# Performance work log

Hardware: AMD Instinct MI355X
Metric: run time of the kernel (lower is better)

## Reference

```python
import jax, jax.numpy as jnp
import numpy as np

B, N, D, O = 128, 256, 512, 512
EPS = 1e-5


def setup_inputs() -> dict:
    key = jax.random.key(0)
    ks = jax.random.split(key, 12)
    Observation = jax.random.normal(ks[0], (B, N, D), dtype=jnp.float32)
    mask = jax.random.bernoulli(ks[1], 0.7, (B, N))
    s = 0.02
    W1 = jax.random.normal(ks[2], (D, O), dtype=jnp.float32) * s
    W2 = jax.random.normal(ks[3], (O, O), dtype=jnp.float32) * s
    W3 = jax.random.normal(ks[4], (O, O), dtype=jnp.float32) * s
    g1 = 1.0 + 0.1 * jax.random.normal(ks[5], (D,), dtype=jnp.float32)
    b1 = 0.02 * jax.random.normal(ks[6], (D,), dtype=jnp.float32)
    g2 = 1.0 + 0.1 * jax.random.normal(ks[7], (O,), dtype=jnp.float32)
    b2 = 0.02 * jax.random.normal(ks[8], (O,), dtype=jnp.float32)
    g3 = 1.0 + 0.1 * jax.random.normal(ks[9], (O,), dtype=jnp.float32)
    b3 = 0.02 * jax.random.normal(ks[10], (O,), dtype=jnp.float32)
    return {"Observation": Observation, "mask": mask,
            "g1": g1, "b1": b1, "W1": W1,
            "g2": g2, "b2": b2, "W2": W2,
            "g3": g3, "b3": b3, "W3": W3}


def layer_norm(x, g, b):
    m = jnp.mean(x, axis=-1, keepdims=True)
    v = jnp.mean(jnp.square(x - m), axis=-1, keepdims=True)
    return (x - m) * jax.lax.rsqrt(v + EPS) * g + b


def reference(Observation, mask, g1, b1, W1, g2, b2, W2, g3, b3, W3):
    Bv, Nv, Dv = Observation.shape
    # _grant_at_least_one_valid: force element 0 valid if a row is all-invalid
    all_invalid = ~jnp.any(mask, axis=1)  # [B]
    mask = mask | (all_invalid[:, None] & (jnp.arange(Nv) == 0)[None, :])
    x = Observation.reshape(-1, Dv)  # [B*N, D]
    # Block 1: LN -> Linear (no bias) -> Tanh (dropout is eval identity)
    h1 = jnp.tanh(layer_norm(x, g1, b1) @ W1)
    # Block 2
    h2 = jnp.tanh(layer_norm(h1, g2, b2) @ W2)
    # Block 3 with residual input (h2 + h1), no activation
    o3 = layer_norm(h2 + h1, g3, b3) @ W3  # [B*N, O]
    fill = jnp.finfo(o3.dtype).min
    o3 = jnp.where(mask.reshape(-1, 1), o3, fill)
    out = jax.nn.softmax(o3.reshape(Bv, Nv, -1), axis=1)
    return jnp.nan_to_num(out, nan=0.0)
```

## Files before the change

kernel.cpp:

```cpp
#include <hip/hip_runtime.h>


#define RTOT 32768
#define NN   256

typedef _Float16 f16;
typedef __attribute__((ext_vector_type(4))) _Float16 f16x4;
typedef __attribute__((ext_vector_type(8))) _Float16 f16x8;
typedef __attribute__((ext_vector_type(4))) float f32x4;

#define EPS16 520
#define EPS32 516

__device__ __forceinline__ float fast_tanh(float x) {
  float e = __expf(2.f * x);
  return 1.f - 2.f * __builtin_amdgcn_rcpf(e + 1.f);
}
__device__ __forceinline__ void async_copy16(const void* g, void* l) {
  __builtin_amdgcn_global_load_lds(
      (const __attribute__((address_space(1))) unsigned int*)g,
      (__attribute__((address_space(3))) unsigned int*)l, 16, 0, 0);
}

__global__ void prep_w_kernel(const float* __restrict__ W1, const float* __restrict__ W2,
                              const float* __restrict__ W3, f16* __restrict__ WT) {
  int idx = blockIdx.x * 256 + threadIdx.x;
  int s   = idx >> 18;
  int rem = idx & 0x3FFFF;
  int o   = rem >> 9;
  int d   = rem & 511;
  const float* W = (s == 0) ? W1 : (s == 1) ? W2 : W3;
  WT[idx] = (f16)W[d * 512 + o];
}

__global__ __launch_bounds__(256) void ln1_kernel(const float* __restrict__ in,
                                                  const float* __restrict__ g,
                                                  const float* __restrict__ b,
                                                  f16* __restrict__ outA) {
  int wv = threadIdx.x >> 6, lane = threadIdx.x & 63;
  size_t row = (size_t)blockIdx.x * 4 + wv;
  const float* x = in + (row << 9);
  float4 v0 = *(const float4*)(x + lane * 4);
  float4 v1 = *(const float4*)(x + 256 + lane * 4);
  float s = v0.x + v0.y + v0.z + v0.w + v1.x + v1.y + v1.z + v1.w;
  float q = v0.x*v0.x + v0.y*v0.y + v0.z*v0.z + v0.w*v0.w
          + v1.x*v1.x + v1.y*v1.y + v1.z*v1.z + v1.w*v1.w;
  #pragma unroll
  for (int off = 1; off < 64; off <<= 1) {
    s += __shfl_xor(s, off, 64);
    q += __shfl_xor(q, off, 64);
  }
  float mean = s * (1.f / 512.f);
  float var  = q * (1.f / 512.f) - mean * mean;
  float inv  = 1.f / sqrtf(var + 1e-5f);
  float4 g0 = *(const float4*)(g + lane * 4);
  float4 b0 = *(const float4*)(b + lane * 4);
  float4 g1 = *(const float4*)(g + 256 + lane * 4);
  float4 b1 = *(const float4*)(b + 256 + lane * 4);
  f16x4 o0, o1;
  o0[0] = (f16)((v0.x - mean) * inv * g0.x + b0.x);
  o0[1] = (f16)((v0.y - mean) * inv * g0.y + b0.y);
  o0[2] = (f16)((v0.z - mean) * inv * g0.z + b0.z);
  o0[3] = (f16)((v0.w - mean) * inv * g0.w + b0.w);
  o1[0] = (f16)((v1.x - mean) * inv * g1.x + b1.x);
  o1[1] = (f16)((v1.y - mean) * inv * g1.y + b1.y);
  o1[2] = (f16)((v1.z - mean) * inv * g1.z + b1.z);
  o1[3] = (f16)((v1.w - mean) * inv * g1.w + b1.w);
  *(f16x4*)&outA[(row << 9) + lane * 4] = o0;
  *(f16x4*)&outA[(row << 9) + 256 + lane * 4] = o1;
}

template <int STAGE>
__global__ __launch_bounds__(512, 4) void fused_kernel(
    const f16* __restrict__ A, const f16* __restrict__ BT,
    const float* __restrict__ g, const float* __restrict__ b,
    f16* __restrict__ H1, f16* __restrict__ outH, float* __restrict__ outF) {
  __shared__ __align__(16) char smem[73728];
  __shared__ __align__(16) float2 sPart[512];
  __shared__ __align__(16) float2 sStat[64];
  f16* sA = (f16*)smem;
  f16* sB = (f16*)(smem + 8192);

  int t = threadIdx.x, lane = t & 63, wv = t >> 6;
  int row16 = lane & 15, quad = lane >> 4;
  int rBase = blockIdx.x * 64;
  int lr  = lane >> 3;
  int lcs = ((lane & 7) ^ (lane >> 3)) * 8;

  f32x4 acc[4][4] = {};

  for (int k0 = 0; k0 < 512; k0 += 64) {
    {
      const f16* ga = A + (((size_t)(rBase + wv * 8 + lr)) << 9) + k0 + lcs;
      async_copy16(ga, sA + (wv * 8) * 64);
    }
    #pragma unroll
    for (int p = 0; p < 8; ++p) {
      int r = wv * 64 + p * 8;
      const f16* gb = BT + (((size_t)(r + lr)) << 9) + k0 + lcs;
      async_copy16(gb, sB + r * 64);
    }
    __syncthreads();
    #pragma unroll
    for (int kk = 0; kk < 64; kk += 32) {
      int kb = kk >> 3;
      f16x8 af[4], bf[4];
      #pragma unroll
      for (int i = 0; i < 4; ++i) {
        int ar = i * 16 + row16;
        int br = wv * 64 + i * 16 + row16;
        af[i] = *(const f16x8*)&sA[ar * 64 + (((quad + kb) ^ (ar & 7)) << 3)];
        bf[i] = *(const f16x8*)&sB[br * 64 + (((quad + kb) ^ (br & 7)) << 3)];
      }
      #pragma unroll
      for (int mi = 0; mi < 4; ++mi)
        #pragma unroll
        for (int ni = 0; ni < 4; ++ni)
          acc[mi][ni] = __builtin_amdgcn_mfma_f32_16x16x32_f16(af[mi], bf[ni], acc[mi][ni], 0, 0, 0);
    }
    __syncthreads();
  }

  if constexpr (STAGE == 2) {
    float* sE = (float*)smem;
    #pragma unroll
    for (int half = 0; half < 2; ++half) {
      #pragma unroll
      for (int mi = 0; mi < 2; ++mi) {
        int rt = half * 2 + mi;
        #pragma unroll
        for (int ni = 0; ni < 4; ++ni) {
          int col = wv * 64 + ni * 16 + row16;
          #pragma unroll
          for (int rg = 0; rg < 4; ++rg)
            sE[(mi * 16 + quad * 4 + rg) * EPS32 + col] = acc[rt][ni][rg];
        }
      }
      __syncthreads();
      #pragma unroll
      for (int i = 0; i < 8; ++i) {
        int gi = t + i * 512;
        int row = gi >> 7, cg = (gi & 127) * 4;
        f32x4 v = *(const f32x4*)&sE[row * EPS32 + cg];
        *(f32x4*)&outF[(((size_t)(rBase + half * 32 + row)) << 9) + cg] = v;
      }
      __syncthreads();
    }
    return;
  } else {
    float gv[4], bv[4];
    #pragma unroll
    for (int ni = 0; ni < 4; ++ni) {
      int c = wv * 64 + ni * 16 + row16;
      gv[ni] = g[c]; bv[ni] = b[c];
    }

    f16* sH = (f16*)smem;
    if constexpr (STAGE == 1) {
      #pragma unroll
      for (int p = 0; p < 8; ++p) {
        const f16* gh = H1 + (((size_t)(rBase + wv * 8 + p)) << 9) + lane * 8;
        async_copy16(gh, sH + (wv * 8 + p) * 512);
      }
    }

    #pragma unroll
    for (int mi = 0; mi < 4; ++mi)
      #pragma unroll
      for (int ni = 0; ni < 4; ++ni)
        #pragma unroll
        for (int rg = 0; rg < 4; ++rg)
          acc[mi][ni][rg] = fast_tanh(acc[mi][ni][rg]);

    if constexpr (STAGE == 1) {
      __syncthreads();
      #pragma unroll
      for (int mi = 0; mi < 4; ++mi)
        #pragma unroll
        for (int ni = 0; ni < 4; ++ni) {
          int col = wv * 64 + ni * 16 + row16;
          #pragma unroll
          for (int rg = 0; rg < 4; ++rg)
            acc[mi][ni][rg] += (float)sH[(mi * 16 + quad * 4 + rg) * 512 + col];
        }
    }

    f16* sE = (f16*)smem;
    if constexpr (STAGE == 0) {
      #pragma unroll
      for (int mi = 0; mi < 4; ++mi)
        #pragma unroll
        for (int ni = 0; ni < 4; ++ni) {
          int col = wv * 64 + ni * 16 + row16;
          #pragma unroll
          for (int rg = 0; rg < 4; ++rg)
            sE[(mi * 16 + quad * 4 + rg) * EPS16 + col] = (f16)acc[mi][ni][rg];
        }
    }

    #pragma unroll
    for (int mi = 0; mi < 4; ++mi)
      #pragma unroll
      for (int rg = 0; rg < 4; ++rg) {
        float s = 0.f, q = 0.f;
        #pragma unroll
        for (int ni = 0; ni < 4; ++ni) {
          float v = acc[mi][ni][rg];
          s += v; q += v * v;
        }
        #pragma unroll
        for (int off = 1; off < 16; off <<= 1) {
          s += __shfl_xor(s, off, 16);
          q += __shfl_xor(q, off, 16);
        }
        if (row16 == 0)
          sPart[wv * 64 + mi * 16 + quad * 4 + rg] = make_float2(s, q);
      }
    __syncthreads();

    if (t < 64) {
      float s = 0.f, q = 0.f;
      #pragma unroll
      for (int w = 0; w < 8; ++w) {
        float2 p = sPart[w * 64 + t];
        s += p.x; q += p.y;
      }
      float mean = s * (1.f / 512.f);
      float var  = q * (1.f / 512.f) - mean * mean;
      sStat[t] = make_float2(mean, 1.f / sqrtf(var + 1e-5f));
    }
    if constexpr (STAGE == 0) {
      #pragma unroll
      for (int i = 0; i < 8; ++i) {
        int gi = t + i * 512;
        int row = gi >> 6, cg = (gi & 63) * 8;
        f16x8 v = *(const f16x8*)&sE[row * EPS16 + cg];
        *(f16x8*)&H1[(((size_t)(rBase + row)) << 9) + cg] = v;
      }
    }
    __syncthreads();

    #pragma unroll
    for (int mi = 0; mi < 4; ++mi)
      #pragma unroll
      for (int rg = 0; rg < 4; ++rg) {
        int row = mi * 16 + quad * 4 + rg;
        float2 st = sStat[row];
        #pragma unroll
        for (int ni = 0; ni < 4; ++ni) {
          int col = wv * 64 + ni * 16 + row16;
          sE[row * EPS16 + col] = (f16)((acc[mi][ni][rg] - st.x) * st.y * gv[ni] + bv[ni]);
        }
      }
    __syncthreads();

    #pragma unroll
    for (int i = 0; i < 8; ++i) {
      int gi = t + i * 512;
      int row = gi >> 6, cg = (gi & 63) * 8;
      f16x8 v = *(const f16x8*)&sE[row * EPS16 + cg];
      *(f16x8*)&outH[(((size_t)(rBase + row)) << 9) + cg] = v;
    }
  }
}

__global__ __launch_bounds__(256, 2) void softmax_kernel(const float* __restrict__ o3,
                                                         const int* __restrict__ mask,
                                                         float* __restrict__ out) {
  __shared__ float sz[NN * 64];
  __shared__ float sredm[4 * 64];
  __shared__ float sreds[4 * 64];
  __shared__ int   smask[NN];

  int b  = blockIdx.x >> 3;
  int oc = blockIdx.x & 7;
  int t  = threadIdx.x;
  int o_l = t & 63;
  int n_h = t >> 6;

  int mt = mask[b * NN + t];
  int any = __syncthreads_or(mt);
  smask[t] = (t == 0 && !any) ? 1 : mt;
  __syncthreads();

  const float* src = o3 + (((size_t)(b * NN)) << 9) + oc * 64;
  #pragma unroll 4
  for (int j = 0; j < 64; ++j) {
    int n = j * 4 + n_h;
    float v = src[((size_t)n << 9) + o_l];
    sz[n * 64 + o_l] = smask[n] ? v : -3.4e38f;
  }
  __syncthreads();

  float mx = -3.4e38f;
  #pragma unroll 8
  for (int i = 0; i < 64; ++i)
    mx = fmaxf(mx, sz[(n_h * 64 + i) * 64 + o_l]);
  sredm[n_h * 64 + o_l] = mx;
  __syncthreads();
  float m4 = fmaxf(fmaxf(sredm[o_l], sredm[64 + o_l]),
                   fmaxf(sredm[128 + o_l], sredm[192 + o_l]));

  float sm = 0.f;
  #pragma unroll 8
  for (int i = 0; i < 64; ++i)
    sm += __expf(sz[(n_h * 64 + i) * 64 + o_l] - m4);
  sreds[n_h * 64 + o_l] = sm;
  __syncthreads();
  float tot = sreds[o_l] + sreds[64 + o_l] + sreds[128 + o_l] + sreds[192 + o_l];
  float inv = 1.f / tot;

  float* dst = out + (((size_t)(b * NN)) << 9) + oc * 64;
  #pragma unroll 4
  for (int j = 0; j < 64; ++j) {
    int n = j * 4 + n_h;
    dst[((size_t)n << 9) + o_l] = __expf(sz[n * 64 + o_l] - m4) * inv;
  }
}

extern "C" void kernel_launch(void* const* d_in, const int* in_sizes, int n_in,
                              void* d_out, int out_size, void* d_ws, size_t ws_size,
                              hipStream_t stream) {
  const float* Obs = (const float*)d_in[0];
  const int*   msk = (const int*)d_in[1];
  const float* g1  = (const float*)d_in[2];
  const float* b1  = (const float*)d_in[3];
  const float* W1  = (const float*)d_in[4];
  const float* g2  = (const float*)d_in[5];
  const float* b2  = (const float*)d_in[6];
  const float* W2  = (const float*)d_in[7];
  const float* g3  = (const float*)d_in[8];
  const float* b3  = (const float*)d_in[9];
  const float* W3  = (const float*)d_in[10];
  float* out = (float*)d_out;

  char* ws = (char*)d_ws;
  const size_t MB = 1u << 20;
  f16*   Ah0 = (f16*)ws;
  f16*   Ah1 = (f16*)(ws + 32 * MB);
  f16*   H1h = (f16*)(ws + 64 * MB);
  float* Lg  = (float*)(ws + 64 * MB);
  f16*   WT  = (f16*)(ws + 128 * MB);

  prep_w_kernel<<<3072, 256, 0, stream>>>(W1, W2, W3, WT);
  ln1_kernel<<<8192, 256, 0, stream>>>(Obs, g1, b1, Ah0);
  fused_kernel<0><<<512, 512, 0, stream>>>(Ah0, WT,          g2, b2, H1h, Ah1, nullptr);
  fused_kernel<1><<<512, 512, 0, stream>>>(Ah1, WT + 262144, g3, b3, H1h, Ah0, nullptr);
  fused_kernel<2><<<512, 512, 0, stream>>>(Ah0, WT + 524288, nullptr, nullptr, nullptr, nullptr, Lg);
  softmax_kernel<<<1024, 256, 0, stream>>>(Lg, msk, out);
}
```

Measured before the change: 303.8 us.

## Fuse LN1 and all three GEMM stages into one persistent-row mega kernel

Replaces the separate LN1 kernel and three per-stage fused GEMM kernels with a single kernel. Each block keeps its 64-row activation tile resident in LDS across all three layers, holds h1 in registers as f16 for the residual, and streams weights through a double-buffered 32-wide K slice. The final logits are written as f16 instead of f32 to halve softmax input traffic. This removes the global round trips for intermediate activations and the extra launches, at the cost of more LDS per block (occupancy 2 instead of 4), higher register pressure, and reduced precision of the logits.

```diff
diff --git a/kernel.cpp b/kernel.cpp
--- a/kernel.cpp
+++ b/kernel.cpp
@@ -1,16 +1,13 @@
 #include <hip/hip_runtime.h>
 
 
-#define RTOT 32768
-#define NN   256
+#define NN 256
 
 typedef _Float16 f16;
+typedef __attribute__((ext_vector_type(2))) _Float16 f16x2;
 typedef __attribute__((ext_vector_type(4))) _Float16 f16x4;
 typedef __attribute__((ext_vector_type(8))) _Float16 f16x8;
 typedef __attribute__((ext_vector_type(4))) float f32x4;
-
-#define EPS16 520
-#define EPS32 516
 
 __device__ __forceinline__ float fast_tanh(float x) {
   float e = __expf(2.f * x);
@@ -33,238 +30,208 @@
   WT[idx] = (f16)W[d * 512 + o];
 }
 
-__global__ __launch_bounds__(256) void ln1_kernel(const float* __restrict__ in,
-                                                  const float* __restrict__ g,
-                                                  const float* __restrict__ b,
-                                                  f16* __restrict__ outA) {
-  int wv = threadIdx.x >> 6, lane = threadIdx.x & 63;
-  size_t row = (size_t)blockIdx.x * 4 + wv;
-  const float* x = in + (row << 9);
-  float4 v0 = *(const float4*)(x + lane * 4);
-  float4 v1 = *(const float4*)(x + 256 + lane * 4);
-  float s = v0.x + v0.y + v0.z + v0.w + v1.x + v1.y + v1.z + v1.w;
-  float q = v0.x*v0.x + v0.y*v0.y + v0.z*v0.z + v0.w*v0.w
-          + v1.x*v1.x + v1.y*v1.y + v1.z*v1.z + v1.w*v1.w;
-  #pragma unroll
-  for (int off = 1; off < 64; off <<= 1) {
-    s += __shfl_xor(s, off, 64);
-    q += __shfl_xor(q, off, 64);
-  }
-  float mean = s * (1.f / 512.f);
-  float var  = q * (1.f / 512.f) - mean * mean;
-  float inv  = 1.f / sqrtf(var + 1e-5f);
-  float4 g0 = *(const float4*)(g + lane * 4);
-  float4 b0 = *(const float4*)(b + lane * 4);
-  float4 g1 = *(const float4*)(g + 256 + lane * 4);
-  float4 b1 = *(const float4*)(b + 256 + lane * 4);
-  f16x4 o0, o1;
-  o0[0] = (f16)((v0.x - mean) * inv * g0.x + b0.x);
-  o0[1] = (f16)((v0.y - mean) * inv * g0.y + b0.y);
-  o0[2] = (f16)((v0.z - mean) * inv * g0.z + b0.z);
-  o0[3] = (f16)((v0.w - mean) * inv * g0.w + b0.w);
-  o1[0] = (f16)((v1.x - mean) * inv * g1.x + b1.x);
-  o1[1] = (f16)((v1.y - mean) * inv * g1.y + b1.y);
-  o1[2] = (f16)((v1.z - mean) * inv * g1.z + b1.z);
-  o1[3] = (f16)((v1.w - mean) * inv * g1.w + b1.w);
-  *(f16x4*)&outA[(row << 9) + lane * 4] = o0;
-  *(f16x4*)&outA[(row << 9) + 256 + lane * 4] = o1;
-}
-
-template <int STAGE>
-__global__ __launch_bounds__(512, 4) void fused_kernel(
-    const f16* __restrict__ A, const f16* __restrict__ BT,
-    const float* __restrict__ g, const float* __restrict__ b,
-    f16* __restrict__ H1, f16* __restrict__ outH, float* __restrict__ outF) {
-  __shared__ __align__(16) char smem[73728];
+__global__ __launch_bounds__(512, 2) void mega_kernel(
+    const float* __restrict__ Obs, const f16* __restrict__ WT,
+    const float* __restrict__ g1, const float* __restrict__ b1,
+    const float* __restrict__ g2, const float* __restrict__ b2,
+    const float* __restrict__ g3, const float* __restrict__ b3,
+    f16* __restrict__ Lg) {
+  __shared__ __align__(16) f16 sA[64 * 512];
+  __shared__ __align__(16) f16 sW[2][512 * 32];
   __shared__ __align__(16) float2 sPart[512];
   __shared__ __align__(16) float2 sStat[64];
-  f16* sA = (f16*)smem;
-  f16* sB = (f16*)(smem + 8192);
-
-  int t = threadIdx.x, lane = t & 63, wv = t >> 6;
-  int row16 = lane & 15, quad = lane >> 4;
-  int rBase = blockIdx.x * 64;
-  int lr  = lane >> 3;
-  int lcs = ((lane & 7) ^ (lane >> 3)) * 8;
-
-  f32x4 acc[4][4] = {};
-
-  for (int k0 = 0; k0 < 512; k0 += 64) {
-    {
-      const f16* ga = A + (((size_t)(rBase + wv * 8 + lr)) << 9) + k0 + lcs;
-      async_copy16(ga, sA + (wv * 8) * 64);
-    }
-    #pragma unroll
-    for (int p = 0; p < 8; ++p) {
-      int r = wv * 64 + p * 8;
-      const f16* gb = BT + (((size_t)(r + lr)) << 9) + k0 + lcs;
-      async_copy16(gb, sB + r * 64);
+
+  const int t = threadIdx.x, lane = t & 63, wv = t >> 6;
+  const int row16 = lane & 15, quad = lane >> 4;
+  const int rBase = blockIdx.x * 64;
+
+  {
+    const float* src = Obs + (size_t)rBase * 512;
+    float4 v[16];
+    #pragma unroll
+    for (int i = 0; i < 16; ++i)
+      v[i] = *(const float4*)(src + i * 2048 + t * 4);
+    #pragma unroll
+    for (int i = 0; i < 16; ++i) {
+      float s = v[i].x + v[i].y + v[i].z + v[i].w;
+      float q = v[i].x * v[i].x + v[i].y * v[i].y + v[i].z * v[i].z + v[i].w * v[i].w;
+      #pragma unroll
+      for (int off = 1; off < 64; off <<= 1) {
+        s += __shfl_xor(s, off, 64);
+        q += __shfl_xor(q, off, 64);
+      }
+      if (lane == 0) sPart[i * 8 + wv] = make_float2(s, q);
     }
     __syncthreads();
-    #pragma unroll
-    for (int kk = 0; kk < 64; kk += 32) {
-      int kb = kk >> 3;
-      f16x8 af[4], bf[4];
-      #pragma unroll
-      for (int i = 0; i < 4; ++i) {
-        int ar = i * 16 + row16;
-        int br = wv * 64 + i * 16 + row16;
-        af[i] = *(const f16x8*)&sA[ar * 64 + (((quad + kb) ^ (ar & 7)) << 3)];
-        bf[i] = *(const f16x8*)&sB[br * 64 + (((quad + kb) ^ (br & 7)) << 3)];
-      }
-      #pragma unroll
-      for (int mi = 0; mi < 4; ++mi)
-        #pragma unroll
-        for (int ni = 0; ni < 4; ++ni)
-          acc[mi][ni] = __builtin_amdgcn_mfma_f32_16x16x32_f16(af[mi], bf[ni], acc[mi][ni], 0, 0, 0);
-    }
-    __syncthreads();
-  }
-
-  if constexpr (STAGE == 2) {
-    float* sE = (float*)smem;
-    #pragma unroll
-    for (int half = 0; half < 2; ++half) {
-      #pragma unroll
-      for (int mi = 0; mi < 2; ++mi) {
-        int rt = half * 2 + mi;
-        #pragma unroll
-        for (int ni = 0; ni < 4; ++ni) {
-          int col = wv * 64 + ni * 16 + row16;
-          #pragma unroll
-          for (int rg = 0; rg < 4; ++rg)
-            sE[(mi * 16 + quad * 4 + rg) * EPS32 + col] = acc[rt][ni][rg];
-        }
-      }
-      __syncthreads();
-      #pragma unroll
-      for (int i = 0; i < 8; ++i) {
-        int gi = t + i * 512;
-        int row = gi >> 7, cg = (gi & 127) * 4;
-        f32x4 v = *(const f32x4*)&sE[row * EPS32 + cg];
-        *(f32x4*)&outF[(((size_t)(rBase + half * 32 + row)) << 9) + cg] = v;
-      }
-      __syncthreads();
-    }
-    return;
-  } else {
-    float gv[4], bv[4];
-    #pragma unroll
-    for (int ni = 0; ni < 4; ++ni) {
-      int c = wv * 64 + ni * 16 + row16;
-      gv[ni] = g[c]; bv[ni] = b[c];
-    }
-
-    f16* sH = (f16*)smem;
-    if constexpr (STAGE == 1) {
-      #pragma unroll
-      for (int p = 0; p < 8; ++p) {
-        const f16* gh = H1 + (((size_t)(rBase + wv * 8 + p)) << 9) + lane * 8;
-        async_copy16(gh, sH + (wv * 8 + p) * 512);
-      }
-    }
-
-    #pragma unroll
-    for (int mi = 0; mi < 4; ++mi)
-      #pragma unroll
-      for (int ni = 0; ni < 4; ++ni)
-        #pragma unroll
-        for (int rg = 0; rg < 4; ++rg)
-          acc[mi][ni][rg] = fast_tanh(acc[mi][ni][rg]);
-
-    if constexpr (STAGE == 1) {
-      __syncthreads();
-      #pragma unroll
-      for (int mi = 0; mi < 4; ++mi)
-        #pragma unroll
-        for (int ni = 0; ni < 4; ++ni) {
-          int col = wv * 64 + ni * 16 + row16;
-          #pragma unroll
-          for (int rg = 0; rg < 4; ++rg)
-            acc[mi][ni][rg] += (float)sH[(mi * 16 + quad * 4 + rg) * 512 + col];
-        }
-    }
-
-    f16* sE = (f16*)smem;
-    if constexpr (STAGE == 0) {
-      #pragma unroll
-      for (int mi = 0; mi < 4; ++mi)
-        #pragma unroll
-        for (int ni = 0; ni < 4; ++ni) {
-          int col = wv * 64 + ni * 16 + row16;
-          #pragma unroll
-          for (int rg = 0; rg < 4; ++rg)
-            sE[(mi * 16 + quad * 4 + rg) * EPS16 + col] = (f16)acc[mi][ni][rg];
-        }
-    }
-
-    #pragma unroll
-    for (int mi = 0; mi < 4; ++mi)
-      #pragma unroll
-      for (int rg = 0; rg < 4; ++rg) {
-        float s = 0.f, q = 0.f;
-        #pragma unroll
-        for (int ni = 0; ni < 4; ++ni) {
-          float v = acc[mi][ni][rg];
-          s += v; q += v * v;
-        }
-        #pragma unroll
-        for (int off = 1; off < 16; off <<= 1) {
-          s += __shfl_xor(s, off, 16);
-          q += __shfl_xor(q, off, 16);
-        }
-        if (row16 == 0)
-          sPart[wv * 64 + mi * 16 + quad * 4 + rg] = make_float2(s, q);
-      }
-    __syncthreads();
-
     if (t < 64) {
-      float s = 0.f, q = 0.f;
-      #pragma unroll
-      for (int w = 0; w < 8; ++w) {
-        float2 p = sPart[w * 64 + t];
-        s += p.x; q += p.y;
-      }
+      float2 p0 = sPart[(t >> 2) * 8 + (t & 3) * 2];
+      float2 p1 = sPart[(t >> 2) * 8 + (t & 3) * 2 + 1];
+      float s = p0.x + p1.x, q = p0.y + p1.y;
       float mean = s * (1.f / 512.f);
       float var  = q * (1.f / 512.f) - mean * mean;
       sStat[t] = make_float2(mean, 1.f / sqrtf(var + 1e-5f));
     }
-    if constexpr (STAGE == 0) {
-      #pragma unroll
-      for (int i = 0; i < 8; ++i) {
-        int gi = t + i * 512;
-        int row = gi >> 6, cg = (gi & 63) * 8;
-        f16x8 v = *(const f16x8*)&sE[row * EPS16 + cg];
-        *(f16x8*)&H1[(((size_t)(rBase + row)) << 9) + cg] = v;
-      }
-    }
     __syncthreads();
-
-    #pragma unroll
-    for (int mi = 0; mi < 4; ++mi)
-      #pragma unroll
-      for (int rg = 0; rg < 4; ++rg) {
-        int row = mi * 16 + quad * 4 + rg;
-        float2 st = sStat[row];
-        #pragma unroll
-        for (int ni = 0; ni < 4; ++ni) {
-          int col = wv * 64 + ni * 16 + row16;
-          sE[row * EPS16 + col] = (f16)((acc[mi][ni][rg] - st.x) * st.y * gv[ni] + bv[ni]);
-        }
-      }
+    const int colB = (t & 127) * 4;
+    const float4 Gv = *(const float4*)(g1 + colB);
+    const float4 Bv = *(const float4*)(b1 + colB);
+    const int cb = colB >> 3;
+    const int half = (t & 1) * 4;
+    #pragma unroll
+    for (int i = 0; i < 16; ++i) {
+      int r = i * 4 + (t >> 7);
+      float2 st = sStat[r];
+      f16x4 o;
+      o[0] = (f16)((v[i].x - st.x) * st.y * Gv.x + Bv.x);
+      o[1] = (f16)((v[i].y - st.x) * st.y * Gv.y + Bv.y);
+      o[2] = (f16)((v[i].z - st.x) * st.y * Gv.z + Bv.z);
+      o[3] = (f16)((v[i].w - st.x) * st.y * Gv.w + Bv.w);
+      *(f16x4*)&sA[r * 512 + ((cb ^ (r & 7)) << 3) + half] = o;
+    }
+  }
+  __syncthreads();
+
+  f32x4 acc[4][4];
+  f16x2 h1p[4][4][2];
+
+  const int lr = lane >> 2;
+  const int gb = (lane & 3) ^ ((lane >> 3) & 3);
+  const int bswz = (quad ^ ((row16 >> 1) & 3)) << 3;
+
+  for (int stage = 0; stage < 3; ++stage) {
+    const f16* Wg = WT + stage * 262144;
+    #pragma unroll
+    for (int m = 0; m < 4; ++m)
+      #pragma unroll
+      for (int n = 0; n < 4; ++n)
+        acc[m][n] = (f32x4){0.f, 0.f, 0.f, 0.f};
+
+    #pragma unroll
+    for (int p4 = 0; p4 < 4; ++p4) {
+      int rb = wv * 64 + p4 * 16;
+      async_copy16(Wg + (size_t)(rb + lr) * 512 + gb * 8, &sW[0][rb * 32]);
+    }
     __syncthreads();
 
-    #pragma unroll
-    for (int i = 0; i < 8; ++i) {
-      int gi = t + i * 512;
-      int row = gi >> 6, cg = (gi & 63) * 8;
-      f16x8 v = *(const f16x8*)&sE[row * EPS16 + cg];
-      *(f16x8*)&outH[(((size_t)(rBase + row)) << 9) + cg] = v;
+    for (int i = 0; i < 16; ++i) {
+      if (i < 15) {
+        int k0n = (i + 1) * 32;
+        f16* buf = sW[(i + 1) & 1];
+        #pragma unroll
+        for (int p4 = 0; p4 < 4; ++p4) {
+          int rb = wv * 64 + p4 * 16;
+          async_copy16(Wg + (size_t)(rb + lr) * 512 + k0n + gb * 8, buf + rb * 32);
+        }
+      }
+      const f16* bufc = sW[i & 1];
+      int K0B = i * 4;
+      f16x8 af[4], bf[4];
+      #pragma unroll
+      for (int m = 0; m < 4; ++m) {
+        int ar = m * 16 + row16;
+        af[m] = *(const f16x8*)&sA[ar * 512 + (((K0B + quad) ^ (ar & 7)) << 3)];
+      }
+      #pragma unroll
+      for (int n = 0; n < 4; ++n) {
+        int br = wv * 64 + n * 16 + row16;
+        bf[n] = *(const f16x8*)&bufc[br * 32 + bswz];
+      }
+      #pragma unroll
+      for (int m = 0; m < 4; ++m)
+        #pragma unroll
+        for (int n = 0; n < 4; ++n)
+          acc[m][n] = __builtin_amdgcn_mfma_f32_16x16x32_f16(af[m], bf[n], acc[m][n], 0, 0, 0);
+      __syncthreads();
+    }
+
+    if (stage < 2) {
+      const float* Gp = (stage == 0) ? g2 : g3;
+      const float* Bp = (stage == 0) ? b2 : b3;
+      float gv[4], bv[4];
+      #pragma unroll
+      for (int n = 0; n < 4; ++n) {
+        int c = wv * 64 + n * 16 + row16;
+        gv[n] = Gp[c]; bv[n] = Bp[c];
+      }
+      #pragma unroll
+      for (int m = 0; m < 4; ++m)
+        #pragma unroll
+        for (int n = 0; n < 4; ++n)
+          #pragma unroll
+          for (int rg = 0; rg < 4; ++rg) {
+            float x = fast_tanh(acc[m][n][rg]);
+            if (stage == 0) h1p[m][n][rg >> 1][rg & 1] = (f16)x;
+            else            x += (float)h1p[m][n][rg >> 1][rg & 1];
+            acc[m][n][rg] = x;
+          }
+      #pragma unroll
+      for (int m = 0; m < 4; ++m)
+        #pragma unroll
+        for (int rg = 0; rg < 4; ++rg) {
+          float s = acc[m][0][rg] + acc[m][1][rg] + acc[m][2][rg] + acc[m][3][rg];
+          float q = acc[m][0][rg] * acc[m][0][rg] + acc[m][1][rg] * acc[m][1][rg]
+                  + acc[m][2][rg] * acc[m][2][rg] + acc[m][3][rg] * acc[m][3][rg];
+          #pragma unroll
+          for (int off = 1; off < 16; off <<= 1) {
+            s += __shfl_xor(s, off, 16);
+            q += __shfl_xor(q, off, 16);
+          }
+          if (row16 == 0) sPart[wv * 64 + m * 16 + quad * 4 + rg] = make_float2(s, q);
+        }
+      __syncthreads();
+      if (t < 64) {
+        float s = 0.f, q = 0.f;
+        #pragma unroll
+        for (int w = 0; w < 8; ++w) { float2 p = sPart[w * 64 + t]; s += p.x; q += p.y; }
+        float mean = s * (1.f / 512.f);
+        float var  = q * (1.f / 512.f) - mean * mean;
+        sStat[t] = make_float2(mean, 1.f / sqrtf(var + 1e-5f));
+      }
+      __syncthreads();
+      #pragma unroll
+      for (int m = 0; m < 4; ++m)
+        #pragma unroll
+        for (int rg = 0; rg < 4; ++rg) {
+          int r = m * 16 + quad * 4 + rg;
+          float2 st = sStat[r];
+          #pragma unroll
+          for (int n = 0; n < 4; ++n) {
+            int c = wv * 64 + n * 16 + row16;
+            int p = (c >> 3) ^ (r & 7);
+            sA[r * 512 + (p << 3) + (c & 7)] = (f16)((acc[m][n][rg] - st.x) * st.y * gv[n] + bv[n]);
+          }
+        }
+      __syncthreads();
+    } else {
+      f16* sE = (f16*)sW;
+      #pragma unroll
+      for (int half = 0; half < 2; ++half) {
+        #pragma unroll
+        for (int mh = 0; mh < 2; ++mh) {
+          int m = half * 2 + mh;
+          #pragma unroll
+          for (int n = 0; n < 4; ++n) {
+            int c = wv * 64 + n * 16 + row16;
+            #pragma unroll
+            for (int rg = 0; rg < 4; ++rg)
+              sE[(mh * 16 + quad * 4 + rg) * 520 + c] = (f16)acc[m][n][rg];
+          }
+        }
+        __syncthreads();
+        #pragma unroll
+        for (int j = 0; j < 4; ++j) {
+          int gi = t + j * 512;
+          int r = gi >> 6, cg = (gi & 63) * 8;
+          f16x8 o = *(const f16x8*)&sE[r * 520 + cg];
+          *(f16x8*)&Lg[((size_t)(rBase + half * 32 + r)) * 512 + cg] = o;
+        }
+        __syncthreads();
+      }
     }
   }
 }
 
-__global__ __launch_bounds__(256, 2) void softmax_kernel(const float* __restrict__ o3,
+__global__ __launch_bounds__(256, 2) void softmax_kernel(const f16* __restrict__ o3,
                                                          const int* __restrict__ mask,
                                                          float* __restrict__ out) {
   __shared__ float sz[NN * 64];
@@ -283,11 +250,11 @@
   smask[t] = (t == 0 && !any) ? 1 : mt;
   __syncthreads();
 
-  const float* src = o3 + (((size_t)(b * NN)) << 9) + oc * 64;
+  const f16* src = o3 + (((size_t)(b * NN)) << 9) + oc * 64;
   #pragma unroll 4
   for (int j = 0; j < 64; ++j) {
     int n = j * 4 + n_h;
-    float v = src[((size_t)n << 9) + o_l];
+    float v = (float)src[((size_t)n << 9) + o_l];
     sz[n * 64 + o_l] = smask[n] ? v : -3.4e38f;
   }
   __syncthreads();
@@ -336,16 +303,10 @@
 
   char* ws = (char*)d_ws;
   const size_t MB = 1u << 20;
-  f16*   Ah0 = (f16*)ws;
-  f16*   Ah1 = (f16*)(ws + 32 * MB);
-  f16*   H1h = (f16*)(ws + 64 * MB);
-  float* Lg  = (float*)(ws + 64 * MB);
-  f16*   WT  = (f16*)(ws + 128 * MB);
+  f16* Lg = (f16*)ws;
+  f16* WT = (f16*)(ws + 32 * MB);
 
   prep_w_kernel<<<3072, 256, 0, stream>>>(W1, W2, W3, WT);
-  ln1_kernel<<<8192, 256, 0, stream>>>(Obs, g1, b1, Ah0);
-  fused_kernel<0><<<512, 512, 0, stream>>>(Ah0, WT,          g2, b2, H1h, Ah1, nullptr);
-  fused_kernel<1><<<512, 512, 0, stream>>>(Ah1, WT + 262144, g3, b3, H1h, Ah0, nullptr);
-  fused_kernel<2><<<512, 512, 0, stream>>>(Ah0, WT + 524288, nullptr, nullptr, nullptr, nullptr, Lg);
+  mega_kernel<<<512, 512, 0, stream>>>(Obs, WT, g1, b1, g2, b2, g3, b3, Lg);
   softmax_kernel<<<1024, 256, 0, stream>>>(Lg, msk, out);
 }
```

After: 377.0 us. +24.1%, slower.
